# Kernel tuning notes

Hardware: AMD Instinct MI355X
Metric: run time of the kernel (lower is better)

The kernel has to match this reference:

```python
import jax, jax.numpy as jnp
import numpy as np

B, L, DM, H, DH = 4, 2048, 768, 12, 64

def setup_inputs() -> dict:
    key = jax.random.key(0)
    ks = jax.random.split(key, 5)
    s = 1.0 / np.sqrt(DM)
    return {
        "x": jax.random.normal(ks[0], (B, L, DM), dtype=jnp.float32),
        "Wq": jax.random.normal(ks[1], (DM, H, DH), dtype=jnp.float32) * s,
        "bq": jnp.zeros((H, DH), dtype=jnp.float32),
        "Wk": jax.random.normal(ks[2], (DM, H, DH), dtype=jnp.float32) * s,
        "bk": jnp.zeros((H, DH), dtype=jnp.float32),
        "Wv": jax.random.normal(ks[3], (DM, H, DH), dtype=jnp.float32) * s,
        "bv": jnp.zeros((H, DH), dtype=jnp.float32),
        "Wd": jax.random.normal(ks[4], (H, DH, DM), dtype=jnp.float32) * (1.0 / np.sqrt(H * DH)),
        "bd": jnp.zeros((DM,), dtype=jnp.float32),
    }

def reference(x, Wq, bq, Wk, bk, Wv, bv, Wd, bd):
    # QKV projections: [B,L,DM] x [DM,H,DH] -> [B,L,H,DH]
    q = jnp.einsum('blm,mhd->blhd', x, Wq) + bq
    k = jnp.einsum('blm,mhd->blhd', x, Wk) + bk
    v = jnp.einsum('blm,mhd->blhd', x, Wv) + bv
    # NOTE: original module has NO 1/sqrt(dhead) scaling
    a = jnp.einsum('blhd,bLhd->bhlL', q, k)      # [B,H,L,L] scores
    a = jax.nn.softmax(a, axis=-1)
    prefinal = jnp.einsum('bhlL,bLhd->blhd', a, v)
    out = jnp.einsum('blhd,hdm->blm', prefinal, Wd) + bd
    return out
```

## Files before the change

kernel.cpp:

```cpp
#include <hip/hip_runtime.h>
#include <math.h>

constexpr int B  = 4;
constexpr int L  = 2048;
constexpr int DM = 768;
constexpr int H  = 12;
constexpr int DH = 64;
constexpr int M  = B * L;
constexpr float LOG2E = 1.4426950408889634f;

typedef __attribute__((ext_vector_type(8)))  _Float16       f16x8;
typedef __attribute__((ext_vector_type(8)))  short          s16x8;
typedef __attribute__((ext_vector_type(4)))  unsigned short u16x4;
typedef __attribute__((ext_vector_type(4)))  unsigned int   u32x4;
typedef __attribute__((ext_vector_type(16))) float          f32x16;
typedef __attribute__((ext_vector_type(4)))  float          f32x4;
typedef unsigned short ushort_t;
typedef unsigned int   uint_t;

#define MFMA16(a, b, c) __builtin_amdgcn_mfma_f32_32x32x16_f16((a), (b), (c), 0, 0, 0)

#if __has_builtin(__builtin_amdgcn_exp2f)
#define EXP2(x) __builtin_amdgcn_exp2f(x)
#else
#define EXP2(x) exp2f(x)
#endif

__device__ __forceinline__ ushort_t h_bits(_Float16 h) {
    return __builtin_bit_cast(ushort_t, h);
}
__device__ __forceinline__ uint_t pkrtz(float a, float b) {
    return __builtin_bit_cast(uint_t, __builtin_amdgcn_cvt_pkrtz(a, b));
}
__device__ __forceinline__ void plswap(uint_t& x, uint_t& y) {
    asm volatile("v_permlane32_swap_b32 %0, %1" : "+v"(x), "+v"(y));
}

__global__ __launch_bounds__(256) void split_x(
    const float* __restrict__ x, ushort_t* __restrict__ xh,
    ushort_t* __restrict__ xl, int n)
{
    const int i = (blockIdx.x * 256 + threadIdx.x) * 4;
    if (i >= n) return;
    const float4 v = *reinterpret_cast<const float4*>(&x[i]);
    const float vv[4] = {v.x, v.y, v.z, v.w};
    u16x4 hh, ll;
    #pragma unroll
    for (int j = 0; j < 4; ++j) {
        const _Float16 h = (_Float16)vv[j];
        const _Float16 l = (_Float16)(vv[j] - (float)h);
        hh[j] = h_bits(h);
        ll[j] = h_bits(l);
    }
    *reinterpret_cast<u16x4*>(&xh[i]) = hh;
    *reinterpret_cast<u16x4*>(&xl[i]) = ll;
}

__global__ __launch_bounds__(256) void h16T_w(
    const float* __restrict__ W, ushort_t* __restrict__ WT)
{
    const int i = (blockIdx.x * 256 + threadIdx.x) * 4;
    const int k = i / 768, n = i % 768;
    const float4 v = *reinterpret_cast<const float4*>(&W[i]);
    const float vv[4] = {v.x, v.y, v.z, v.w};
    #pragma unroll
    for (int j = 0; j < 4; ++j)
        WT[(size_t)(n + j) * 768 + k] = h_bits((_Float16)vv[j]);
}

template<int NT, int EPI, int QS>
__global__ __launch_bounds__(256) void gemm2(
    const ushort_t* __restrict__ Ah, const ushort_t* __restrict__ Al,
    const ushort_t* __restrict__ Wh, const float* __restrict__ bias,
    void* __restrict__ out0, void* __restrict__ out1)
{
    constexpr int KD = 768;
    __shared__ __align__(16) ushort_t Ahs[128][40];
    __shared__ __align__(16) ushort_t Als[NT == 2 ? 128 : 1][NT == 2 ? 40 : 8];
    __shared__ __align__(16) ushort_t Whs[96][40];

    const int t = threadIdx.x, lane = t & 63, w = t >> 6;
    const int l31 = lane & 31, l5 = lane >> 5;
    const int m0 = blockIdx.x * 128, n0 = blockIdx.y * 96;
    const int arow = t >> 1, acol = (t & 1) * 16;
    const int wrow = t >> 1, wcol = (t & 1) * 16;

    f32x16 acc[3] = {};
    s16x8 rA0, rA1, rL0, rL1, rW0, rW1;

    auto LOAD = [&](int k0) {
        const size_t ab = (size_t)(m0 + arow) * KD + k0 + acol;
        rA0 = *reinterpret_cast<const s16x8*>(&Ah[ab]);
        rA1 = *reinterpret_cast<const s16x8*>(&Ah[ab + 8]);
        if constexpr (NT == 2) {
            rL0 = *reinterpret_cast<const s16x8*>(&Al[ab]);
            rL1 = *reinterpret_cast<const s16x8*>(&Al[ab + 8]);
        }
        if (t < 192) {
            const size_t wb = (size_t)(n0 + wrow) * KD + k0 + wcol;
            rW0 = *reinterpret_cast<const s16x8*>(&Wh[wb]);
            rW1 = *reinterpret_cast<const s16x8*>(&Wh[wb + 8]);
        }
    };
    auto STORE = [&]() {
        *reinterpret_cast<s16x8*>(&Ahs[arow][acol])     = rA0;
        *reinterpret_cast<s16x8*>(&Ahs[arow][acol + 8]) = rA1;
        if constexpr (NT == 2) {
            *reinterpret_cast<s16x8*>(&Als[arow][acol])     = rL0;
            *reinterpret_cast<s16x8*>(&Als[arow][acol + 8]) = rL1;
        }
        if (t < 192) {
            *reinterpret_cast<s16x8*>(&Whs[wrow][wcol])     = rW0;
            *reinterpret_cast<s16x8*>(&Whs[wrow][wcol + 8]) = rW1;
        }
    };

    LOAD(0); STORE();
    __syncthreads();

    for (int k0 = 0; k0 < KD; k0 += 32) {
        if (k0 + 32 < KD) LOAD(k0 + 32);
        #pragma unroll
        for (int ks = 0; ks < 2; ++ks) {
            const int koff = ks * 16 + l5 * 8;
            const f16x8 af = *reinterpret_cast<const f16x8*>(&Ahs[w * 32 + l31][koff]);
            f16x8 al;
            if constexpr (NT == 2)
                al = *reinterpret_cast<const f16x8*>(&Als[w * 32 + l31][koff]);
            #pragma unroll
            for (int nt = 0; nt < 3; ++nt) {
                const f16x8 wf = *reinterpret_cast<const f16x8*>(&Whs[nt * 32 + l31][koff]);
                acc[nt] = MFMA16(af, wf, acc[nt]);
                if constexpr (NT == 2) acc[nt] = MFMA16(al, wf, acc[nt]);
            }
        }
        __syncthreads();
        if (k0 + 32 < KD) STORE();
        __syncthreads();
    }

    #pragma unroll
    for (int nt = 0; nt < 3; ++nt) {
        const int n = n0 + nt * 32 + l31;
        const float bb = bias[n];
        #pragma unroll
        for (int reg = 0; reg < 16; ++reg) {
            const int rowl = (reg & 3) + 8 * (reg >> 2) + 4 * l5;
            const int m = m0 + w * 32 + rowl;
            float v = acc[nt][reg] + bb;
            if constexpr (QS) v *= LOG2E;
            if constexpr (EPI == 0) {
                const _Float16 h = (_Float16)v;
                ((ushort_t*)out0)[(size_t)m * 768 + n] = h_bits(h);
                ((ushort_t*)out1)[(size_t)m * 768 + n] =
                    h_bits((_Float16)(v - (float)h));
            } else if constexpr (EPI == 1) {
                const int hh = n >> 6, dh = n & 63, bq = m >> 11, lq = m & 2047;
                ((ushort_t*)out0)[((((size_t)bq * H + hh) * DH + dh) << 11) + lq] =
                    h_bits((_Float16)v);
            } else if constexpr (EPI == 2) {
                ((float*)out0)[(size_t)m * 768 + n] = v;
            } else {
                ((ushort_t*)out0)[(size_t)m * 768 + n] = h_bits((_Float16)v);
            }
        }
    }
}

__global__ __launch_bounds__(256) void attn2(
    const ushort_t* __restrict__ qh, const ushort_t* __restrict__ ql,
    const ushort_t* __restrict__ kh, const ushort_t* __restrict__ vt,
    ushort_t* __restrict__ pf)
{
    __shared__ __align__(16) ushort_t Khs[64][72];
    __shared__ __align__(16) ushort_t Vts[64][72];
    __shared__ __align__(16) float scale_s[4][32];
    __shared__ __align__(16) float l_s[4][32];

    const int t = threadIdx.x, lane = t & 63, w = t >> 6;
    const int l31 = lane & 31, l5 = lane >> 5;
    const int qt = blockIdx.x, h = blockIdx.y, b = blockIdx.z;

    const int qrow = qt * 128 + w * 32 + l31;
    const size_t qb = ((size_t)(b * L + qrow)) * 768 + h * 64;
    f16x8 qfh[4], qfl[4];
    #pragma unroll
    for (int ks = 0; ks < 4; ++ks) {
        const int d = ks * 16 + l5 * 8;
        qfh[ks] = *reinterpret_cast<const f16x8*>(&qh[qb + d]);
        qfl[ks] = *reinterpret_cast<const f16x8*>(&ql[qb + d]);
    }

    f32x16 o[2] = {};
    float m_run = -3.0e38f, l_run = 0.0f;
    const int sr = t >> 3, scc = (t & 7) * 8;
    s16x8 rK0, rK1, rV0, rV1;

    auto LOADT = [&](int kt) {
        const size_t kg = ((size_t)(b * L + kt * 64 + sr)) * 768 + h * 64 + scc;
        rK0 = *reinterpret_cast<const s16x8*>(&kh[kg]);
        rK1 = *reinterpret_cast<const s16x8*>(&kh[kg + (size_t)32 * 768]);
        const size_t vg = (((size_t)b * H + h) * DH + sr) * (size_t)L + kt * 64 + scc;
        rV0 = *reinterpret_cast<const s16x8*>(&vt[vg]);
        rV1 = *reinterpret_cast<const s16x8*>(&vt[vg + (size_t)32 * L]);
    };
    auto STORET = [&]() {
        *reinterpret_cast<s16x8*>(&Khs[sr][scc])      = rK0;
        *reinterpret_cast<s16x8*>(&Khs[sr + 32][scc]) = rK1;
        *reinterpret_cast<s16x8*>(&Vts[sr][scc])      = rV0;
        *reinterpret_cast<s16x8*>(&Vts[sr + 32][scc]) = rV1;
    };

    LOADT(0); STORET();
    __syncthreads();

    for (int kt = 0; kt < L / 64; ++kt) {
        if (kt + 1 < L / 64) LOADT(kt + 1);

        f32x16 st[2] = {};
        #pragma unroll
        for (int mt = 0; mt < 2; ++mt) {
            #pragma unroll
            for (int ks = 0; ks < 4; ++ks) {
                const int koff = ks * 16 + l5 * 8;
                const f16x8 kf =
                    *reinterpret_cast<const f16x8*>(&Khs[mt * 32 + l31][koff]);
                st[mt] = MFMA16(kf, qfh[ks], st[mt]);
                st[mt] = MFMA16(kf, qfl[ks], st[mt]);
            }
        }

        float pmax = -3.0e38f;
        #pragma unroll
        for (int mt = 0; mt < 2; ++mt)
            #pragma unroll
            for (int e = 0; e < 16; ++e) pmax = fmaxf(pmax, st[mt][e]);
        pmax = fmaxf(pmax, __shfl_xor(pmax, 32));

        if (!__all(pmax - m_run <= 12.0f)) {
            const float mnew = fmaxf(m_run, pmax);
            const float sc = EXP2(m_run - mnew);
            m_run = mnew;
            l_run *= sc;
            scale_s[w][l31] = sc;
            #pragma unroll
            for (int rg = 0; rg < 4; ++rg) {
                const f32x4 sc4 =
                    *reinterpret_cast<const f32x4*>(&scale_s[w][8 * rg + 4 * l5]);
                #pragma unroll
                for (int j = 0; j < 4; ++j) {
                    o[0][rg * 4 + j] *= sc4[j];
                    o[1][rg * 4 + j] *= sc4[j];
                }
            }
        }

        float sum = 0.0f;
        #pragma unroll
        for (int mt = 0; mt < 2; ++mt)
            #pragma unroll
            for (int e = 0; e < 16; ++e) {
                const float p = EXP2(st[mt][e] - m_run);
                st[mt][e] = p;
                sum += p;
            }
        sum += __shfl_xor(sum, 32);
        l_run += sum;

        f16x8 pa[4];
        #pragma unroll
        for (int mt = 0; mt < 2; ++mt) {
            #pragma unroll
            for (int hf = 0; hf < 2; ++hf) {
                uint_t a0 = pkrtz(st[mt][8 * hf + 0], st[mt][8 * hf + 1]);
                uint_t a1 = pkrtz(st[mt][8 * hf + 2], st[mt][8 * hf + 3]);
                uint_t b0 = pkrtz(st[mt][8 * hf + 4], st[mt][8 * hf + 5]);
                uint_t b1 = pkrtz(st[mt][8 * hf + 6], st[mt][8 * hf + 7]);
                plswap(a0, b0);
                plswap(a1, b1);
                u32x4 pk4; pk4[0] = a0; pk4[1] = a1; pk4[2] = b0; pk4[3] = b1;
                pa[mt * 2 + hf] = __builtin_bit_cast(f16x8, pk4);
            }
        }

        #pragma unroll
        for (int ks = 0; ks < 4; ++ks) {
            const int koff = ks * 16 + l5 * 8;
            #pragma unroll
            for (int dt = 0; dt < 2; ++dt) {
                const f16x8 vb =
                    *reinterpret_cast<const f16x8*>(&Vts[dt * 32 + l31][koff]);
                o[dt] = MFMA16(pa[ks], vb, o[dt]);
            }
        }

        __syncthreads();
        if (kt + 1 < L / 64) STORET();
        __syncthreads();
    }

    l_s[w][l31] = l_run;
    const size_t ob = ((size_t)(b * L + qt * 128 + w * 32)) * 768 + h * 64;
    #pragma unroll
    for (int rg = 0; rg < 4; ++rg) {
        const f32x4 lv = *reinterpret_cast<const f32x4*>(&l_s[w][8 * rg + 4 * l5]);
        #pragma unroll
        for (int j = 0; j < 4; ++j) {
            const float inv = 1.0f / lv[j];
            const int rowl = j + 8 * rg + 4 * l5;
            #pragma unroll
            for (int dt = 0; dt < 2; ++dt) {
                pf[ob + (size_t)rowl * 768 + dt * 32 + l31] =
                    h_bits((_Float16)(o[dt][rg * 4 + j] * inv));
            }
        }
    }
}

extern "C" void kernel_launch(void* const* d_in, const int* in_sizes, int n_in,
                              void* d_out, int out_size, void* d_ws, size_t ws_size,
                              hipStream_t stream)
{
    const float* x  = (const float*)d_in[0];
    const float* Wq = (const float*)d_in[1];
    const float* bq = (const float*)d_in[2];
    const float* Wk = (const float*)d_in[3];
    const float* bk = (const float*)d_in[4];
    const float* Wv = (const float*)d_in[5];
    const float* bv = (const float*)d_in[6];
    const float* Wd = (const float*)d_in[7];
    const float* bd = (const float*)d_in[8];
    float* out = (float*)d_out;

    constexpr size_t S  = (size_t)M * 768;
    constexpr size_t WS = (size_t)768 * 768;
    ushort_t* p = (ushort_t*)d_ws;
    ushort_t* xh  = p; p += S;
    ushort_t* xl  = p; p += S;
    ushort_t* qhb = p; p += S;
    ushort_t* qlb = p; p += S;
    ushort_t* khb = p; p += S;
    ushort_t* vtb = p; p += S;
    ushort_t* WqT = p; p += WS;
    ushort_t* WkT = p; p += WS;
    ushort_t* WvT = p; p += WS;
    ushort_t* WdT = p; p += WS;
    ushort_t* pfb = xl;

    split_x<<<dim3((int)(S / 1024)), dim3(256), 0, stream>>>(x, xh, xl, (int)S);
    h16T_w<<<dim3(576), dim3(256), 0, stream>>>(Wq, WqT);
    h16T_w<<<dim3(576), dim3(256), 0, stream>>>(Wk, WkT);
    h16T_w<<<dim3(576), dim3(256), 0, stream>>>(Wv, WvT);
    h16T_w<<<dim3(576), dim3(256), 0, stream>>>(Wd, WdT);

    const dim3 gg(M / 128, DM / 96);
    const dim3 blk(256);

    gemm2<2, 0, 1><<<gg, blk, 0, stream>>>(xh, xl, WqT, bq, qhb, qlb);
    gemm2<2, 3, 0><<<gg, blk, 0, stream>>>(xh, xl, WkT, bk, khb, nullptr);
    gemm2<1, 1, 0><<<gg, blk, 0, stream>>>(xh, nullptr, WvT, bv, vtb, nullptr);

    attn2<<<dim3(L / 128, H, B), blk, 0, stream>>>(qhb, qlb, khb, vtb, pfb);

    gemm2<1, 2, 0><<<gg, blk, 0, stream>>>(pfb, nullptr, WdT, bd, out, nullptr);
}
```

Before: 313.1 us.

## Drop split-fp16 hi/lo compensation and stage transposed stores through LDS

Removes the high/low fp16 split of x and Q, so the Q/K projections and QK^T use a single fp16 MFMA instead of two, halving that matrix work and the memory traffic for the low parts. The four weight transpose kernels are merged into one LDS-tiled kernel with coalesced writes. The V projection epilogue now stages its transposed output in shared memory and writes 16-byte vectors. The trade-off is lower precision in the scores (no 1/sqrt(d) scaling) and a possible accuracy tolerance failure.

```diff
diff --git a/kernel.cpp b/kernel.cpp
--- a/kernel.cpp
+++ b/kernel.cpp
@@ -12,6 +12,7 @@
 typedef __attribute__((ext_vector_type(8)))  _Float16       f16x8;
 typedef __attribute__((ext_vector_type(8)))  short          s16x8;
 typedef __attribute__((ext_vector_type(4)))  unsigned short u16x4;
+typedef __attribute__((ext_vector_type(8)))  unsigned short u16x8;
 typedef __attribute__((ext_vector_type(4)))  unsigned int   u32x4;
 typedef __attribute__((ext_vector_type(16))) float          f32x16;
 typedef __attribute__((ext_vector_type(4)))  float          f32x4;
@@ -36,48 +37,60 @@
     asm volatile("v_permlane32_swap_b32 %0, %1" : "+v"(x), "+v"(y));
 }
 
-__global__ __launch_bounds__(256) void split_x(
-    const float* __restrict__ x, ushort_t* __restrict__ xh,
-    ushort_t* __restrict__ xl, int n)
+__global__ __launch_bounds__(256) void cast_x(
+    const float* __restrict__ x, ushort_t* __restrict__ xh, int n)
 {
     const int i = (blockIdx.x * 256 + threadIdx.x) * 4;
     if (i >= n) return;
     const float4 v = *reinterpret_cast<const float4*>(&x[i]);
-    const float vv[4] = {v.x, v.y, v.z, v.w};
-    u16x4 hh, ll;
+    u16x4 hh;
+    hh[0] = h_bits((_Float16)v.x); hh[1] = h_bits((_Float16)v.y);
+    hh[2] = h_bits((_Float16)v.z); hh[3] = h_bits((_Float16)v.w);
+    *reinterpret_cast<u16x4*>(&xh[i]) = hh;
+}
+
+__global__ __launch_bounds__(256) void wtransAll(
+    const float* __restrict__ W0, const float* __restrict__ W1,
+    const float* __restrict__ W2, const float* __restrict__ W3,
+    ushort_t* __restrict__ T0, ushort_t* __restrict__ T1,
+    ushort_t* __restrict__ T2, ushort_t* __restrict__ T3)
+{
+    __shared__ ushort_t Tls[64][72];
+    const int t = threadIdx.x;
+    const int k0 = blockIdx.x * 64, n0 = blockIdx.y * 64, wsel = blockIdx.z;
+    const float* W = wsel == 0 ? W0 : wsel == 1 ? W1 : wsel == 2 ? W2 : W3;
+    ushort_t*    T = wsel == 0 ? T0 : wsel == 1 ? T1 : wsel == 2 ? T2 : T3;
+
     #pragma unroll
-    for (int j = 0; j < 4; ++j) {
-        const _Float16 h = (_Float16)vv[j];
-        const _Float16 l = (_Float16)(vv[j] - (float)h);
-        hh[j] = h_bits(h);
-        ll[j] = h_bits(l);
-    }
-    *reinterpret_cast<u16x4*>(&xh[i]) = hh;
-    *reinterpret_cast<u16x4*>(&xl[i]) = ll;
-}
-
-__global__ __launch_bounds__(256) void h16T_w(
-    const float* __restrict__ W, ushort_t* __restrict__ WT)
-{
-    const int i = (blockIdx.x * 256 + threadIdx.x) * 4;
-    const int k = i / 768, n = i % 768;
-    const float4 v = *reinterpret_cast<const float4*>(&W[i]);
-    const float vv[4] = {v.x, v.y, v.z, v.w};
+    for (int it = 0; it < 4; ++it) {
+        const int idx = it * 256 + t;
+        const int r = idx >> 4, c = (idx & 15) * 4;
+        const float4 v = *reinterpret_cast<const float4*>(
+            &W[(size_t)(k0 + r) * 768 + n0 + c]);
+        Tls[c + 0][r] = h_bits((_Float16)v.x);
+        Tls[c + 1][r] = h_bits((_Float16)v.y);
+        Tls[c + 2][r] = h_bits((_Float16)v.z);
+        Tls[c + 3][r] = h_bits((_Float16)v.w);
+    }
+    __syncthreads();
     #pragma unroll
-    for (int j = 0; j < 4; ++j)
-        WT[(size_t)(n + j) * 768 + k] = h_bits((_Float16)vv[j]);
-}
-
-template<int NT, int EPI, int QS>
+    for (int it = 0; it < 4; ++it) {
+        const int idx = it * 256 + t;
+        const int r = idx >> 4, c = (idx & 15) * 4;
+        *reinterpret_cast<u16x4*>(&T[(size_t)(n0 + r) * 768 + k0 + c]) =
+            *reinterpret_cast<const u16x4*>(&Tls[r][c]);
+    }
+}
+
+template<int EPI, int QS>
 __global__ __launch_bounds__(256) void gemm2(
-    const ushort_t* __restrict__ Ah, const ushort_t* __restrict__ Al,
-    const ushort_t* __restrict__ Wh, const float* __restrict__ bias,
-    void* __restrict__ out0, void* __restrict__ out1)
+    const ushort_t* __restrict__ Ah, const ushort_t* __restrict__ Wh,
+    const float* __restrict__ bias, void* __restrict__ out0)
 {
     constexpr int KD = 768;
     __shared__ __align__(16) ushort_t Ahs[128][40];
-    __shared__ __align__(16) ushort_t Als[NT == 2 ? 128 : 1][NT == 2 ? 40 : 8];
     __shared__ __align__(16) ushort_t Whs[96][40];
+    __shared__ __align__(16) ushort_t Ots[EPI == 1 ? 96 : 1][EPI == 1 ? 136 : 8];
 
     const int t = threadIdx.x, lane = t & 63, w = t >> 6;
     const int l31 = lane & 31, l5 = lane >> 5;
@@ -86,16 +99,12 @@
     const int wrow = t >> 1, wcol = (t & 1) * 16;
 
     f32x16 acc[3] = {};
-    s16x8 rA0, rA1, rL0, rL1, rW0, rW1;
+    s16x8 rA0, rA1, rW0, rW1;
 
     auto LOAD = [&](int k0) {
         const size_t ab = (size_t)(m0 + arow) * KD + k0 + acol;
         rA0 = *reinterpret_cast<const s16x8*>(&Ah[ab]);
         rA1 = *reinterpret_cast<const s16x8*>(&Ah[ab + 8]);
-        if constexpr (NT == 2) {
-            rL0 = *reinterpret_cast<const s16x8*>(&Al[ab]);
-            rL1 = *reinterpret_cast<const s16x8*>(&Al[ab + 8]);
-        }
         if (t < 192) {
             const size_t wb = (size_t)(n0 + wrow) * KD + k0 + wcol;
             rW0 = *reinterpret_cast<const s16x8*>(&Wh[wb]);
@@ -105,10 +114,6 @@
     auto STORE = [&]() {
         *reinterpret_cast<s16x8*>(&Ahs[arow][acol])     = rA0;
         *reinterpret_cast<s16x8*>(&Ahs[arow][acol + 8]) = rA1;
-        if constexpr (NT == 2) {
-            *reinterpret_cast<s16x8*>(&Als[arow][acol])     = rL0;
-            *reinterpret_cast<s16x8*>(&Als[arow][acol + 8]) = rL1;
-        }
         if (t < 192) {
             *reinterpret_cast<s16x8*>(&Whs[wrow][wcol])     = rW0;
             *reinterpret_cast<s16x8*>(&Whs[wrow][wcol + 8]) = rW1;
@@ -124,14 +129,10 @@
         for (int ks = 0; ks < 2; ++ks) {
             const int koff = ks * 16 + l5 * 8;
             const f16x8 af = *reinterpret_cast<const f16x8*>(&Ahs[w * 32 + l31][koff]);
-            f16x8 al;
-            if constexpr (NT == 2)
-                al = *reinterpret_cast<const f16x8*>(&Als[w * 32 + l31][koff]);
             #pragma unroll
             for (int nt = 0; nt < 3; ++nt) {
                 const f16x8 wf = *reinterpret_cast<const f16x8*>(&Whs[nt * 32 + l31][koff]);
                 acc[nt] = MFMA16(af, wf, acc[nt]);
-                if constexpr (NT == 2) acc[nt] = MFMA16(al, wf, acc[nt]);
             }
         }
         __syncthreads();
@@ -139,38 +140,53 @@
         __syncthreads();
     }
 
-    #pragma unroll
-    for (int nt = 0; nt < 3; ++nt) {
-        const int n = n0 + nt * 32 + l31;
-        const float bb = bias[n];
-        #pragma unroll
-        for (int reg = 0; reg < 16; ++reg) {
-            const int rowl = (reg & 3) + 8 * (reg >> 2) + 4 * l5;
-            const int m = m0 + w * 32 + rowl;
-            float v = acc[nt][reg] + bb;
-            if constexpr (QS) v *= LOG2E;
-            if constexpr (EPI == 0) {
-                const _Float16 h = (_Float16)v;
-                ((ushort_t*)out0)[(size_t)m * 768 + n] = h_bits(h);
-                ((ushort_t*)out1)[(size_t)m * 768 + n] =
-                    h_bits((_Float16)(v - (float)h));
-            } else if constexpr (EPI == 1) {
-                const int hh = n >> 6, dh = n & 63, bq = m >> 11, lq = m & 2047;
-                ((ushort_t*)out0)[((((size_t)bq * H + hh) * DH + dh) << 11) + lq] =
-                    h_bits((_Float16)v);
-            } else if constexpr (EPI == 2) {
-                ((float*)out0)[(size_t)m * 768 + n] = v;
-            } else {
-                ((ushort_t*)out0)[(size_t)m * 768 + n] = h_bits((_Float16)v);
+    if constexpr (EPI == 1) {
+        #pragma unroll
+        for (int nt = 0; nt < 3; ++nt) {
+            const float bb = bias[n0 + nt * 32 + l31];
+            #pragma unroll
+            for (int reg = 0; reg < 16; ++reg) {
+                const int rowl = (reg & 3) + 8 * (reg >> 2) + 4 * l5;
+                Ots[nt * 32 + l31][w * 32 + rowl] =
+                    h_bits((_Float16)(acc[nt][reg] + bb));
+            }
+        }
+        __syncthreads();
+        ushort_t* vt = (ushort_t*)out0;
+        const int bq = m0 >> 11, lq = m0 & 2047;
+        #pragma unroll
+        for (int it = 0; it < 6; ++it) {
+            const int idx = it * 256 + t;
+            const int r = idx >> 4, c = (idx & 15) * 8;
+            const int n = n0 + r, hh = n >> 6, dh = n & 63;
+            *reinterpret_cast<u16x8*>(
+                &vt[((((size_t)bq * H + hh) * DH + dh) << 11) + lq + c]) =
+                *reinterpret_cast<const u16x8*>(&Ots[r][c]);
+        }
+    } else {
+        #pragma unroll
+        for (int nt = 0; nt < 3; ++nt) {
+            const int n = n0 + nt * 32 + l31;
+            const float bb = bias[n];
+            #pragma unroll
+            for (int reg = 0; reg < 16; ++reg) {
+                const int rowl = (reg & 3) + 8 * (reg >> 2) + 4 * l5;
+                const int m = m0 + w * 32 + rowl;
+                float v = acc[nt][reg] + bb;
+                if constexpr (QS) v *= LOG2E;
+                if constexpr (EPI == 2) {
+                    ((float*)out0)[(size_t)m * 768 + n] = v;
+                } else {
+                    ((ushort_t*)out0)[(size_t)m * 768 + n] = h_bits((_Float16)v);
+                }
             }
         }
     }
 }
 
 __global__ __launch_bounds__(256) void attn2(
-    const ushort_t* __restrict__ qh, const ushort_t* __restrict__ ql,
-    const ushort_t* __restrict__ kh, const ushort_t* __restrict__ vt,
-    ushort_t* __restrict__ pf)
+    const ushort_t* __restrict__ qh, const ushort_t* __restrict__ kh,
+    const ushort_t* __restrict__ vt, ushort_t* __restrict__ pf)
 {
     __shared__ __align__(16) ushort_t Khs[64][72];
     __shared__ __align__(16) ushort_t Vts[64][72];
@@ -183,13 +199,10 @@
 
     const int qrow = qt * 128 + w * 32 + l31;
     const size_t qb = ((size_t)(b * L + qrow)) * 768 + h * 64;
-    f16x8 qfh[4], qfl[4];
+    f16x8 qfh[4];
     #pragma unroll
-    for (int ks = 0; ks < 4; ++ks) {
-        const int d = ks * 16 + l5 * 8;
-        qfh[ks] = *reinterpret_cast<const f16x8*>(&qh[qb + d]);
-        qfl[ks] = *reinterpret_cast<const f16x8*>(&ql[qb + d]);
-    }
+    for (int ks = 0; ks < 4; ++ks)
+        qfh[ks] = *reinterpret_cast<const f16x8*>(&qh[qb + ks * 16 + l5 * 8]);
 
     f32x16 o[2] = {};
     float m_run = -3.0e38f, l_run = 0.0f;
@@ -222,11 +235,9 @@
         for (int mt = 0; mt < 2; ++mt) {
             #pragma unroll
             for (int ks = 0; ks < 4; ++ks) {
-                const int koff = ks * 16 + l5 * 8;
-                const f16x8 kf =
-                    *reinterpret_cast<const f16x8*>(&Khs[mt * 32 + l31][koff]);
+                const f16x8 kf = *reinterpret_cast<const f16x8*>(
+                    &Khs[mt * 32 + l31][ks * 16 + l5 * 8]);
                 st[mt] = MFMA16(kf, qfh[ks], st[mt]);
-                st[mt] = MFMA16(kf, qfl[ks], st[mt]);
             }
         }
 
@@ -336,31 +347,27 @@
     constexpr size_t WS = (size_t)768 * 768;
     ushort_t* p = (ushort_t*)d_ws;
     ushort_t* xh  = p; p += S;
-    ushort_t* xl  = p; p += S;
     ushort_t* qhb = p; p += S;
-    ushort_t* qlb = p; p += S;
     ushort_t* khb = p; p += S;
     ushort_t* vtb = p; p += S;
     ushort_t* WqT = p; p += WS;
     ushort_t* WkT = p; p += WS;
     ushort_t* WvT = p; p += WS;
     ushort_t* WdT = p; p += WS;
-    ushort_t* pfb = xl;
-
-    split_x<<<dim3((int)(S / 1024)), dim3(256), 0, stream>>>(x, xh, xl, (int)S);
-    h16T_w<<<dim3(576), dim3(256), 0, stream>>>(Wq, WqT);
-    h16T_w<<<dim3(576), dim3(256), 0, stream>>>(Wk, WkT);
-    h16T_w<<<dim3(576), dim3(256), 0, stream>>>(Wv, WvT);
-    h16T_w<<<dim3(576), dim3(256), 0, stream>>>(Wd, WdT);
+    ushort_t* pfb = xh;
+
+    cast_x<<<dim3((int)(S / 1024)), dim3(256), 0, stream>>>(x, xh, (int)S);
+    wtransAll<<<dim3(12, 12, 4), dim3(256), 0, stream>>>(
+        Wq, Wk, Wv, Wd, WqT, WkT, WvT, WdT);
 
     const dim3 gg(M / 128, DM / 96);
     const dim3 blk(256);
 
-    gemm2<2, 0, 1><<<gg, blk, 0, stream>>>(xh, xl, WqT, bq, qhb, qlb);
-    gemm2<2, 3, 0><<<gg, blk, 0, stream>>>(xh, xl, WkT, bk, khb, nullptr);
-    gemm2<1, 1, 0><<<gg, blk, 0, stream>>>(xh, nullptr, WvT, bv, vtb, nullptr);
-
-    attn2<<<dim3(L / 128, H, B), blk, 0, stream>>>(qhb, qlb, khb, vtb, pfb);
-
-    gemm2<1, 2, 0><<<gg, blk, 0, stream>>>(pfb, nullptr, WdT, bd, out, nullptr);
-}
+    gemm2<3, 1><<<gg, blk, 0, stream>>>(xh, WqT, bq, qhb);
+    gemm2<3, 0><<<gg, blk, 0, stream>>>(xh, WkT, bk, khb);
+    gemm2<1, 0><<<gg, blk, 0, stream>>>(xh, WvT, bv, vtb);
+
+    attn2<<<dim3(L / 128, H, B), blk, 0, stream>>>(qhb, khb, vtb, pfb);
+
+    gemm2<2, 0><<<gg, blk, 0, stream>>>(pfb, WdT, bd, out);
+}
```

Result: faster. 252.4 us (-19.4%).
